# Performance work log

Hardware: AMD Instinct MI355X
Metric: run time of the kernel (lower is better)

Reference implementation:

```python
import jax, jax.numpy as jnp
import numpy as np

VOCAB = 50000
EMB = 128
REVIEW_COUNT = 200000
B, W, NNEG = 8192, 10, 5


def setup_inputs() -> dict:
    key = jax.random.key(0)
    k1, k2, k3, k4, k5, k6 = jax.random.split(key, 6)
    review_ids = jax.random.randint(k1, (B,), 0, REVIEW_COUNT - 1, dtype=jnp.int32)
    review_word_emb = jax.random.normal(k2, (B, W, EMB), dtype=jnp.float32)
    review_word_mask = jnp.ones((B, W), dtype=jnp.float32)
    # stands in for torch.multinomial(word_dists, B*W*n_negs) in the original forward
    neg_idxs = jax.random.randint(k3, (B, W * NNEG), 0, VOCAB, dtype=jnp.int32)
    word_emb_table = jax.random.normal(k4, (VOCAB, EMB), dtype=jnp.float32)
    review_emb_table = jax.random.normal(k5, (REVIEW_COUNT, EMB), dtype=jnp.float32)
    # padding_idx row is zero, matching nn.Embedding(padding_idx=review_count-1)
    review_emb_table = review_emb_table.at[REVIEW_COUNT - 1].set(0.0)
    return {
        "review_ids": review_ids,
        "review_word_emb": review_word_emb,
        "review_word_mask": review_word_mask,
        "neg_idxs": neg_idxs,
        "word_emb_table": word_emb_table,
        "review_emb_table": review_emb_table,
        "n_negs": NNEG,
    }


def reference(review_ids, review_word_emb, review_word_mask, neg_idxs,
              word_emb_table, review_emb_table, n_negs):
    b, w, e = review_word_emb.shape
    review_emb = review_emb_table[review_ids]            # [B, E]
    neg_emb = word_emb_table[neg_idxs]                   # [B, W*n_negs, E]
    # bmm(review_word_emb, review_emb.unsqueeze(2)) -> per-word dot products
    pos_score = jnp.einsum('bwe,be->bw', review_word_emb, review_emb)       # [B, W]
    neg_score = jnp.einsum('bne,be->bn', neg_emb, review_emb)               # [B, W*n_negs]
    neg_score = neg_score.reshape(b, w, n_negs)                             # [B, W, n_negs]
    # BCEWithLogitsLoss(reduction='none'): target=1 for pos, 0 for neg; sum over (1+n_negs)
    loss_per_word = jax.nn.softplus(-pos_score) + jax.nn.softplus(neg_score).sum(-1)  # [B, W]
    # get_vector_mean: masked mean over window, word_count clamped to >=1
    word_count = jnp.maximum(review_word_mask.sum(-1, keepdims=True), 1.0)  # [B, 1]
    loss = (loss_per_word * review_word_mask).sum(-1, keepdims=True) / word_count  # [B, 1]
    return review_emb, loss
```

## Files before the change

### kernel.cpp

```cpp
#include <hip/hip_runtime.h>
#include <math.h>


__device__ __forceinline__ float stable_softplus(float x) {
    return fmaxf(x, 0.0f) + log1pf(__expf(-fabsf(x)));
}

template<int W, int NN>
__global__ void __launch_bounds__(256, 4)
pv_spec_kernel(const int* __restrict__ review_ids,
               const float* __restrict__ rw_emb,
               const float* __restrict__ mask,
               const int* __restrict__ neg_idxs,
               const float* __restrict__ word_tab,
               const float* __restrict__ rev_tab,
               float* __restrict__ out_rev,
               float* __restrict__ out_loss,
               int B)
{
    constexpr int E  = 128;
    constexpr int WN = W * NN;
    constexpr int ND = W + WN;
    constexpr int NP = (ND + 3) / 4;

    const int wave = threadIdx.x >> 6;
    const int lane = threadIdx.x & 63;
    const int b = blockIdx.x * (blockDim.x >> 6) + wave;
    if (b >= B) return;

    const int sub = lane >> 4;
    const int sl  = lane & 15;

    const int rid = review_ids[b];
    const float4 rv1 = *reinterpret_cast<const float4*>(
        rev_tab + (size_t)rid * E + sl * 4);
    const float4 rv2 = *reinterpret_cast<const float4*>(
        rev_tab + (size_t)rid * E + 64 + sl * 4);

    if (lane < 16) {
        *reinterpret_cast<float4*>(out_rev + (size_t)b * E + lane * 4) = rv1;
    } else if (lane < 32) {
        *reinterpret_cast<float4*>(out_rev + (size_t)b * E + lane * 4) = rv2;
    }

    const int idx_l = (lane < WN) ? neg_idxs[(size_t)b * WN + lane] : 0;
    float md_l = 0.0f;
    if (lane < ND) {
        const int w = (lane < W) ? lane : (lane - W) / NN;
        md_l = mask[(size_t)b * W + w];
    }

    const float* rows[NP];
    float msk[NP];
    #pragma unroll
    for (int p = 0; p < NP; ++p) {
        const int d = p * 4 + sub;
        const bool is_pos = (d < W);
        const bool valid  = (d < ND);
        const int  ni     = __shfl(idx_l, valid ? (is_pos ? 0 : (d - W)) : 0);
        const float m_raw = __shfl(md_l, valid ? d : 0);
        msk[p] = valid ? m_raw : 0.0f;
        rows[p] = is_pos ? rw_emb + ((size_t)b * W + d) * E
                         : word_tab + (size_t)ni * E;
    }

    float acc[NP];
    #pragma unroll
    for (int p = 0; p < NP; ++p) {
        const float4 x1 = *reinterpret_cast<const float4*>(rows[p] + sl * 4);
        const float4 x2 = *reinterpret_cast<const float4*>(rows[p] + 64 + sl * 4);
        float v;
        v = x1.x * rv1.x;
        v = fmaf(x1.y, rv1.y, v);
        v = fmaf(x1.z, rv1.z, v);
        v = fmaf(x1.w, rv1.w, v);
        v = fmaf(x2.x, rv2.x, v);
        v = fmaf(x2.y, rv2.y, v);
        v = fmaf(x2.z, rv2.z, v);
        v = fmaf(x2.w, rv2.w, v);
        acc[p] = v;
    }

    #pragma unroll
    for (int p = 0; p < NP; ++p) {
        float v = acc[p];
        v += __shfl_xor(v, 1);
        v += __shfl_xor(v, 2);
        v += __shfl_xor(v, 4);
        v += __shfl_xor(v, 8);
        acc[p] = v;
    }

    float loss_acc = 0.0f;
    #pragma unroll
    for (int p = 0; p < NP; ++p) {
        const int d = p * 4 + sub;
        const float sgn = (d < W) ? -1.0f : 1.0f;
        loss_acc += msk[p] * stable_softplus(sgn * acc[p]);
    }
    loss_acc = (sl == 0) ? loss_acc : 0.0f;

    float cntv = (lane < W) ? md_l : 0.0f;
    #pragma unroll
    for (int s = 32; s >= 1; s >>= 1) {
        loss_acc += __shfl_xor(loss_acc, s);
        cntv     += __shfl_xor(cntv, s);
    }

    if (lane == 0) {
        out_loss[b] = loss_acc / fmaxf(cntv, 1.0f);
    }
}

__global__ void __launch_bounds__(256, 4)
pv_generic_kernel(const int* __restrict__ review_ids,
                  const float* __restrict__ rw_emb,
                  const float* __restrict__ mask,
                  const int* __restrict__ neg_idxs,
                  const float* __restrict__ word_tab,
                  const float* __restrict__ rev_tab,
                  float* __restrict__ out_rev,
                  float* __restrict__ out_loss,
                  int B, int W, int NN)
{
    const int wave = threadIdx.x >> 6;
    const int lane = threadIdx.x & 63;
    const int b = blockIdx.x * (blockDim.x >> 6) + wave;
    if (b >= B) return;

    const int E   = 128;
    const int sub = lane >> 4;
    const int sl  = lane & 15;
    const int WN  = W * NN;
    const int nd  = W + WN;

    const int rid = review_ids[b];
    const float4 rv1 = *reinterpret_cast<const float4*>(
        rev_tab + (size_t)rid * E + sl * 4);
    const float4 rv2 = *reinterpret_cast<const float4*>(
        rev_tab + (size_t)rid * E + 64 + sl * 4);
    if (lane < 16) {
        *reinterpret_cast<float4*>(out_rev + (size_t)b * E + lane * 4) = rv1;
    } else if (lane < 32) {
        *reinterpret_cast<float4*>(out_rev + (size_t)b * E + lane * 4) = rv2;
    }

    const int idx_l = (lane < WN) ? neg_idxs[(size_t)b * WN + lane] : 0;
    float md_l = 0.0f;
    if (lane < nd) {
        const int w = (lane < W) ? lane : (lane - W) / NN;
        md_l = mask[(size_t)b * W + w];
    }

    float loss_acc = 0.0f;
    const int npass = (nd + 3) >> 2;
    for (int p = 0; p < npass; ++p) {
        const int d = p * 4 + sub;
        const bool is_pos = (d < W);
        const bool valid  = (d < nd);
        const int  ni     = __shfl(idx_l, valid ? (is_pos ? 0 : (d - W)) : 0);
        const float m_raw = __shfl(md_l, valid ? d : 0);
        const float m     = valid ? m_raw : 0.0f;
        const float* row = is_pos ? rw_emb + ((size_t)b * W + d) * E
                                  : word_tab + (size_t)ni * E;
        const float sgn = is_pos ? -1.0f : 1.0f;
        const float4 x1 = *reinterpret_cast<const float4*>(row + sl * 4);
        const float4 x2 = *reinterpret_cast<const float4*>(row + 64 + sl * 4);
        float v;
        v = x1.x * rv1.x;
        v = fmaf(x1.y, rv1.y, v);
        v = fmaf(x1.z, rv1.z, v);
        v = fmaf(x1.w, rv1.w, v);
        v = fmaf(x2.x, rv2.x, v);
        v = fmaf(x2.y, rv2.y, v);
        v = fmaf(x2.z, rv2.z, v);
        v = fmaf(x2.w, rv2.w, v);
        v += __shfl_xor(v, 1);
        v += __shfl_xor(v, 2);
        v += __shfl_xor(v, 4);
        v += __shfl_xor(v, 8);
        const float term = m * stable_softplus(sgn * v);
        loss_acc += (sl == 0) ? term : 0.0f;
    }

    float cntv = (lane < W) ? md_l : 0.0f;
    #pragma unroll
    for (int s = 32; s >= 1; s >>= 1) {
        loss_acc += __shfl_xor(loss_acc, s);
        cntv     += __shfl_xor(cntv, s);
    }
    if (lane == 0) {
        out_loss[b] = loss_acc / fmaxf(cntv, 1.0f);
    }
}

extern "C" void kernel_launch(void* const* d_in, const int* in_sizes, int n_in,
                              void* d_out, int out_size, void* d_ws, size_t ws_size,
                              hipStream_t stream)
{
    const int*   review_ids = (const int*)  d_in[0];
    const float* rw_emb     = (const float*)d_in[1];
    const float* mask       = (const float*)d_in[2];
    const int*   neg_idxs   = (const int*)  d_in[3];
    const float* word_tab   = (const float*)d_in[4];
    const float* rev_tab    = (const float*)d_in[5];

    const int B  = in_sizes[0];
    const int BW = in_sizes[2];
    const int W  = BW / B;
    const int NN = in_sizes[3] / BW;

    float* out_rev  = (float*)d_out;
    float* out_loss = (float*)d_out + (size_t)B * 128;

    const int waves_per_blk = 4;
    const int grid = (B + waves_per_blk - 1) / waves_per_blk;

    if (W == 10 && NN == 5) {
        pv_spec_kernel<10, 5><<<grid, 256, 0, stream>>>(
            review_ids, rw_emb, mask, neg_idxs, word_tab, rev_tab,
            out_rev, out_loss, B);
    } else {
        pv_generic_kernel<<<grid, 256, 0, stream>>>(
            review_ids, rw_emb, mask, neg_idxs, word_tab, rev_tab,
            out_rev, out_loss, B, W, NN);
    }
}
```

Measured before the change: 44.48 us.

## Replace all-loads-upfront with three-deep rolling prefetch and raise occupancy bound

```diff
diff --git a/kernel.cpp b/kernel.cpp
--- a/kernel.cpp
+++ b/kernel.cpp
@@ -7,8 +7,8 @@
 }
 
 template<int W, int NN>
-__global__ void __launch_bounds__(256, 4)
-pv_spec_kernel(const int* __restrict__ review_ids,
+__global__ void __launch_bounds__(256, 8)
+pv_pipe_kernel(const int* __restrict__ review_ids,
                const float* __restrict__ rw_emb,
                const float* __restrict__ mask,
                const int* __restrict__ neg_idxs,
@@ -21,7 +21,8 @@
     constexpr int E  = 128;
     constexpr int WN = W * NN;
     constexpr int ND = W + WN;
-    constexpr int NP = (ND + 3) / 4;
+    constexpr int NP = ND / 4;
+    static_assert(ND % 4 == 0, "specialized kernel needs ND divisible by 4");
 
     const int wave = threadIdx.x >> 6;
     const int lane = threadIdx.x & 63;
@@ -50,25 +51,32 @@
         md_l = mask[(size_t)b * W + w];
     }
 
-    const float* rows[NP];
-    float msk[NP];
+    float4 bufa[3], bufb[3];
+
+    auto issue = [&](int p) {
+        const int d = p * 4 + sub;
+        const bool is_pos = (d < W);
+        const int ni = __shfl(idx_l, is_pos ? 0 : (d - W));
+        const float* row = is_pos ? rw_emb + ((size_t)b * W + d) * E
+                                  : word_tab + (size_t)ni * E;
+        bufa[p % 3] = *reinterpret_cast<const float4*>(row + sl * 4);
+        bufb[p % 3] = *reinterpret_cast<const float4*>(row + 64 + sl * 4);
+    };
+
+    issue(0);
+    issue(1);
+
+    float loss_acc = 0.0f;
     #pragma unroll
     for (int p = 0; p < NP; ++p) {
+        if (p + 2 < NP) issue(p + 2);
+
         const int d = p * 4 + sub;
-        const bool is_pos = (d < W);
-        const bool valid  = (d < ND);
-        const int  ni     = __shfl(idx_l, valid ? (is_pos ? 0 : (d - W)) : 0);
-        const float m_raw = __shfl(md_l, valid ? d : 0);
-        msk[p] = valid ? m_raw : 0.0f;
-        rows[p] = is_pos ? rw_emb + ((size_t)b * W + d) * E
-                         : word_tab + (size_t)ni * E;
-    }
-
-    float acc[NP];
-    #pragma unroll
-    for (int p = 0; p < NP; ++p) {
-        const float4 x1 = *reinterpret_cast<const float4*>(rows[p] + sl * 4);
-        const float4 x2 = *reinterpret_cast<const float4*>(rows[p] + 64 + sl * 4);
+        const float m   = __shfl(md_l, d);
+        const float sgn = (d < W) ? -1.0f : 1.0f;
+
+        const float4 x1 = bufa[p % 3];
+        const float4 x2 = bufb[p % 3];
         float v;
         v = x1.x * rv1.x;
         v = fmaf(x1.y, rv1.y, v);
@@ -78,27 +86,15 @@
         v = fmaf(x2.y, rv2.y, v);
         v = fmaf(x2.z, rv2.z, v);
         v = fmaf(x2.w, rv2.w, v);
-        acc[p] = v;
-    }
-
-    #pragma unroll
-    for (int p = 0; p < NP; ++p) {
-        float v = acc[p];
+
         v += __shfl_xor(v, 1);
         v += __shfl_xor(v, 2);
         v += __shfl_xor(v, 4);
         v += __shfl_xor(v, 8);
-        acc[p] = v;
-    }
-
-    float loss_acc = 0.0f;
-    #pragma unroll
-    for (int p = 0; p < NP; ++p) {
-        const int d = p * 4 + sub;
-        const float sgn = (d < W) ? -1.0f : 1.0f;
-        loss_acc += msk[p] * stable_softplus(sgn * acc[p]);
-    }
-    loss_acc = (sl == 0) ? loss_acc : 0.0f;
+
+        const float term = m * stable_softplus(sgn * v);
+        loss_acc += (sl == 0) ? term : 0.0f;
+    }
 
     float cntv = (lane < W) ? md_l : 0.0f;
     #pragma unroll
@@ -217,7 +213,7 @@
     const int grid = (B + waves_per_blk - 1) / waves_per_blk;
 
     if (W == 10 && NN == 5) {
-        pv_spec_kernel<10, 5><<<grid, 256, 0, stream>>>(
+        pv_pipe_kernel<10, 5><<<grid, 256, 0, stream>>>(
             review_ids, rw_emb, mask, neg_idxs, word_tab, rev_tab,
             out_rev, out_loss, B);
     } else {
```

New measurement: 41.37 us. 1.08x faster.
